# Optimization experiments

Hardware: AMD Instinct MI355X
Metric: run time of the kernel (lower is better)

## Reference

```python
import jax, jax.numpy as jnp
import numpy as np

B, S, H, E, K = 4, 2048, 1024, 8, 2

def setup_inputs() -> dict:
    key = jax.random.key(0)
    ks = jax.random.split(key, 7)
    scale = 1.0 / np.sqrt(H)
    return {
        "hidden_states": jax.random.normal(ks[0], (B, S, H), dtype=jnp.float32),
        "top_k_index": jax.random.randint(ks[1], (B, S, K), 0, E, dtype=jnp.int64),
        "top_k_weights": jax.random.uniform(ks[2], (B, S, K), dtype=jnp.float32),
        "w1": jax.random.normal(ks[3], (E, H, H), dtype=jnp.float32) * scale,
        "b1": jax.random.normal(ks[4], (E, H), dtype=jnp.float32) * scale,
        "w2": jax.random.normal(ks[5], (E, H, H), dtype=jnp.float32) * scale,
        "b2": jax.random.normal(ks[6], (E, H), dtype=jnp.float32) * scale,
    }

def reference(hidden_states, top_k_index, top_k_weights, w1, b1, w2, b2):
    # Per-token, per-expert combine weight: sum over k of tkw * (idx == e) -> [B,S,E]
    match = (top_k_index[..., None] == jnp.arange(E)[None, None, None, :])  # [B,S,K,E]
    comb = jnp.einsum("bsk,bske->bse", top_k_weights, match.astype(top_k_weights.dtype))
    # Dense per-expert FFN over ALL tokens (faithful to the naive module).
    h1 = jax.nn.relu(jnp.einsum("bsh,ehf->ebsf", hidden_states, w1) + b1[:, None, None, :])  # [E,B,S,H]
    h2 = jnp.einsum("ebsh,ehf->ebsf", h1, w2) + b2[:, None, None, :]  # [E,B,S,H]
    # Mask-weighted sum over experts.
    out = jnp.einsum("ebsh,bse->bsh", h2, comb)
    return out
```

## Files before the change

### kernel.cpp

```cpp
#include <hip/hip_runtime.h>
#include <hip/hip_bf16.h>
#include <stdint.h>

#define E_    8
#define H_    1024
#define NTOK  8192
#define KSEL  2
#define NSLOT (NTOK * KSEL)

typedef __attribute__((ext_vector_type(8))) short   short8_t;
typedef __attribute__((ext_vector_type(4))) float   f32x4;

#define BM 160
#define BN 128
#define BK 64
#define MAXMT 110
#define NT    (H_ / BN)
#define NWG   (MAXMT * NT)

#define CNT_OFF   0
#define TOK_OFF   1024
#define WSL_OFF   (TOK_OFF + NSLOT * 4)
#define XB_OFF    (1 << 18)
#define H1_OFF    (XB_OFF + (size_t)NTOK * H_ * 2)
#define W1T_OFF   (H1_OFF + (size_t)(NSLOT + 2048) * H_ * 2)
#define W2T_OFF   (W1T_OFF + (size_t)E_ * H_ * H_ * 2)

#define RT_T 1024
#define RT_S (NSLOT / RT_T)

__global__ __launch_bounds__(RT_T) void route_all(
    const int* __restrict__ idx, const float* __restrict__ tkw,
    int* __restrict__ cnt, int* __restrict__ tok, float* __restrict__ wsl) {
  __shared__ int hist[E_ * RT_T];
  const int t = threadIdx.x;
  const int p0 = t * RT_S;

  int myi[RT_S];
#pragma unroll
  for (int i = 0; i < RT_S; i += 4)
    *(int4*)&myi[i] = *(const int4*)&idx[p0 + i];
  int lc[E_];
#pragma unroll
  for (int j = 0; j < E_; ++j) lc[j] = 0;
#pragma unroll
  for (int i = 0; i < RT_S; ++i)
#pragma unroll
    for (int j = 0; j < E_; ++j) lc[j] += (myi[i] == j) ? 1 : 0;

#pragma unroll
  for (int j = 0; j < E_; ++j) hist[j * RT_T + t] = lc[j];
  __syncthreads();

  for (int s = 1; s < RT_T; s <<= 1) {
    int v[E_];
#pragma unroll
    for (int j = 0; j < E_; ++j) v[j] = (t >= s) ? hist[j * RT_T + (t - s)] : 0;
    __syncthreads();
#pragma unroll
    for (int j = 0; j < E_; ++j) hist[j * RT_T + t] += v[j];
    __syncthreads();
  }

  int tot[E_];
#pragma unroll
  for (int j = 0; j < E_; ++j) tot[j] = hist[j * RT_T + (RT_T - 1)];
  int base[E_];
  {
    int s = 0;
#pragma unroll
    for (int j = 0; j < E_; ++j) { base[j] = s; s += tot[j]; }
  }
  if (t < E_) cnt[t] = tot[t];

  int cur[E_];
#pragma unroll
  for (int j = 0; j < E_; ++j) cur[j] = base[j] + hist[j * RT_T + t] - lc[j];

  float myw[RT_S];
#pragma unroll
  for (int i = 0; i < RT_S; i += 4)
    *(float4*)&myw[i] = *(const float4*)&tkw[p0 + i];
#pragma unroll
  for (int i = 0; i < RT_S; ++i) {
    const int ev = myi[i];
    int pos = 0;
#pragma unroll
    for (int j = 0; j < E_; ++j)
      if (ev == j) { pos = cur[j]; cur[j] = pos + 1; }
    tok[pos] = (p0 + i) >> 1;
    wsl[pos] = myw[i];
  }
}

__global__ void xcast_zero(const float* __restrict__ x, __hip_bfloat16* __restrict__ xb,
                           float* __restrict__ out) {
  const size_t base = ((size_t)blockIdx.x * 256 + threadIdx.x) * 16;
  f32x4 z = f32x4{0.f, 0.f, 0.f, 0.f};
#pragma unroll
  for (int j = 0; j < 4; ++j) *(f32x4*)(out + base + j * 4) = z;
#pragma unroll
  for (int h = 0; h < 2; ++h) {
    f32x4 v0 = *(const f32x4*)(x + base + h * 8);
    f32x4 v1 = *(const f32x4*)(x + base + h * 8 + 4);
    union { __hip_bfloat16 b[8]; uint2 u[2]; } cv;
#pragma unroll
    for (int j = 0; j < 4; ++j) {
      cv.b[j]     = __float2bfloat16(v0[j]);
      cv.b[4 + j] = __float2bfloat16(v1[j]);
    }
    *(uint2*)(xb + base + h * 8)     = cv.u[0];
    *(uint2*)(xb + base + h * 8 + 4) = cv.u[1];
  }
}

__global__ void transpose_cast(const float* __restrict__ w1, const float* __restrict__ w2,
                               __hip_bfloat16* __restrict__ wt1, __hip_bfloat16* __restrict__ wt2) {
  __shared__ __hip_bfloat16 t[64][65];
  const int z = blockIdx.z;
  const float* W = (z < E_ ? w1 : w2) + ((size_t)(z & 7) << 20);
  __hip_bfloat16* WT = (z < E_ ? wt1 : wt2) + ((size_t)(z & 7) << 20);
  const int h0 = blockIdx.y * 64, f0 = blockIdx.x * 64;
  const int tid = threadIdx.x;
  const int tx = tid & 63, ty = tid >> 6;
#pragma unroll
  for (int i = 0; i < 16; ++i) {
    const int hl = i * 4 + ty;
    t[hl][tx] = __float2bfloat16(W[(size_t)(h0 + hl) * H_ + f0 + tx]);
  }
  __syncthreads();
  const int htx = tid & 15;
  const int fy  = tid >> 4;
#pragma unroll
  for (int j = 0; j < 4; ++j) {
    const int f = j * 16 + fy;
    union { __hip_bfloat16 h[4]; uint2 u; } v;
#pragma unroll
    for (int k = 0; k < 4; ++k) v.h[k] = t[htx * 4 + k][f];
    *reinterpret_cast<uint2*>(&WT[(size_t)(f0 + f) * H_ + h0 + htx * 4]) = v.u;
  }
}

#define FENCE_BAR() do {                                   \
    asm volatile("s_waitcnt lgkmcnt(0)" ::: "memory");     \
    __builtin_amdgcn_s_barrier();                          \
    __builtin_amdgcn_sched_barrier(0);                     \
  } while (0)

template <int EPI>
__launch_bounds__(256, 4)
__global__ void moe_gemm(const __hip_bfloat16* __restrict__ Asrc,
                         const __hip_bfloat16* __restrict__ Wt,
                         const float* __restrict__ bias,
                         __hip_bfloat16* __restrict__ h1out,
                         float* __restrict__ out,
                         const int* __restrict__ cnt,
                         const int* __restrict__ tok, const float* __restrict__ wsl) {
  const int wgid = (blockIdx.x & 7) * (NWG / 8) + (blockIdx.x >> 3);
  const int bt = wgid >> 3;
  const int nt = wgid & 7;

  int cn[E_];
#pragma unroll
  for (int i = 0; i < E_; ++i) cn[i] = cnt[i];
  int e = -1, mt = 0, count = 0, arow0 = 0;
  {
    int tacc = 0, sacc = 0;
#pragma unroll
    for (int i = 0; i < E_; ++i) {
      const int nti = (cn[i] + BM - 1) / BM;
      if (e < 0 && bt < tacc + nti) { e = i; mt = bt - tacc; count = cn[i]; arow0 = sacc + mt * BM; }
      tacc += nti; sacc += cn[i];
    }
  }
  if (e < 0) return;
  const size_t Arow0 = (size_t)arow0;

  const int tid = threadIdx.x;
  const int lane = tid & 63;
  const int wid = tid >> 6;
  const int wm = wid >> 1, wn = wid & 1;
  const int l15 = lane & 15, hi = lane >> 4, l7 = lane & 7;

  const __hip_bfloat16* Bexp = Wt + ((size_t)e << 20) + (size_t)(nt * BN) * H_;

  __shared__ __hip_bfloat16 smA[BM * BK];
  __shared__ __hip_bfloat16 smB[BN * BK];

  const int srow = tid >> 3;
  const int sun  = (tid & 7) * 8;
  const int swu  = (((tid & 7) ^ (srow & 7)) * 8);

  const __hip_bfloat16* aptr[5];
#pragma unroll
  for (int i = 0; i < 5; ++i) {
    if constexpr (EPI == 0) {
      int p = arow0 + i * 32 + srow;
      if (p > NSLOT - 1) p = NSLOT - 1;
      aptr[i] = Asrc + (size_t)tok[p] * H_ + sun;
    } else {
      aptr[i] = Asrc + (Arow0 + i * 32 + srow) * H_ + sun;
    }
  }
  const __hip_bfloat16* bptr = Bexp + (size_t)srow * H_ + sun;

  short8_t ra[5], rb[4];

  auto loadreg = [&](int kt) {
#pragma unroll
    for (int i = 0; i < 5; ++i)
      ra[i] = *(const short8_t*)(aptr[i] + kt * BK);
#pragma unroll
    for (int i = 0; i < 4; ++i)
      rb[i] = *(const short8_t*)(bptr + (size_t)(i * 32) * H_ + kt * BK);
  };
  auto dswrite = [&]() {
#pragma unroll
    for (int i = 0; i < 5; ++i)
      *(short8_t*)&smA[(i * 32 + srow) * BK + swu] = ra[i];
#pragma unroll
    for (int i = 0; i < 4; ++i)
      *(short8_t*)&smB[(i * 32 + srow) * BK + swu] = rb[i];
  };

  f32x4 acc[5][4];
#pragma unroll
  for (int mi = 0; mi < 5; ++mi)
#pragma unroll
    for (int ni = 0; ni < 4; ++ni) acc[mi][ni] = f32x4{0.f, 0.f, 0.f, 0.f};

  const int pu[2] = { ((0 * 4 + hi) ^ l7) * 8, ((1 * 4 + hi) ^ l7) * 8 };

  auto compute = [&]() {
#pragma unroll
    for (int ks = 0; ks < 2; ++ks) {
      short8_t a[5], b[4];
#pragma unroll
      for (int mi = 0; mi < 5; ++mi)
        a[mi] = *(const short8_t*)&smA[(wm * 80 + mi * 16 + l15) * BK + pu[ks]];
#pragma unroll
      for (int ni = 0; ni < 4; ++ni)
        b[ni] = *(const short8_t*)&smB[(wn * 64 + ni * 16 + l15) * BK + pu[ks]];
#pragma unroll
      for (int mi = 0; mi < 5; ++mi)
#pragma unroll
        for (int ni = 0; ni < 4; ++ni)
          acc[mi][ni] = __builtin_amdgcn_mfma_f32_16x16x32_bf16(a[mi], b[ni], acc[mi][ni], 0, 0, 0);
    }
  };

  const int KT = H_ / BK;

  loadreg(0);
  dswrite();
  FENCE_BAR();

  for (int kt = 0; kt < KT; ++kt) {
    if (kt + 1 < KT) loadreg(kt + 1);
    compute();
    if (kt + 1 < KT) {
      FENCE_BAR();
      dswrite();
      FENCE_BAR();
    }
  }

  const int colb = nt * BN + wn * 64;
  float bv[4];
#pragma unroll
  for (int ni = 0; ni < 4; ++ni) bv[ni] = bias[e * H_ + colb + ni * 16 + l15];

  if constexpr (EPI == 0) {
#pragma unroll
    for (int mi = 0; mi < 5; ++mi)
#pragma unroll
      for (int r = 0; r < 4; ++r) {
        const int lr = wm * 80 + mi * 16 + hi * 4 + r;
        if (mt * BM + lr < count) {
          __hip_bfloat16* rp = h1out + (Arow0 + lr) * H_ + colb;
#pragma unroll
          for (int ni = 0; ni < 4; ++ni) {
            float v = acc[mi][ni][r] + bv[ni];
            rp[ni * 16 + l15] = __float2bfloat16(fmaxf(v, 0.f));
          }
        }
      }
  } else {
#pragma unroll
    for (int mi = 0; mi < 5; ++mi)
#pragma unroll
      for (int r = 0; r < 4; ++r) {
        const int lr = wm * 80 + mi * 16 + hi * 4 + r;
        if (mt * BM + lr < count) {
          const int p = arow0 + lr;
          float* rp = out + (size_t)tok[p] * H_ + colb;
          const float w = wsl[p];
#pragma unroll
          for (int ni = 0; ni < 4; ++ni)
            atomicAdd(rp + ni * 16 + l15, (acc[mi][ni][r] + bv[ni]) * w);
        }
      }
  }
}

extern "C" void kernel_launch(void* const* d_in, const int* in_sizes, int n_in,
                              void* d_out, int out_size, void* d_ws, size_t ws_size,
                              hipStream_t stream) {
  const float* x   = (const float*)d_in[0];
  const int*   idx = (const int*)d_in[1];
  const float* tkw = (const float*)d_in[2];
  const float* w1  = (const float*)d_in[3];
  const float* b1  = (const float*)d_in[4];
  const float* w2  = (const float*)d_in[5];
  const float* b2  = (const float*)d_in[6];
  float* out = (float*)d_out;

  uint8_t* ws = (uint8_t*)d_ws;
  int*   cnt  = (int*)(ws + CNT_OFF);
  int*   tok  = (int*)(ws + TOK_OFF);
  float* wsl  = (float*)(ws + WSL_OFF);
  __hip_bfloat16* xb  = (__hip_bfloat16*)(ws + XB_OFF);
  __hip_bfloat16* h1  = (__hip_bfloat16*)(ws + H1_OFF);
  __hip_bfloat16* w1t = (__hip_bfloat16*)(ws + W1T_OFF);
  __hip_bfloat16* w2t = (__hip_bfloat16*)(ws + W2T_OFF);

  transpose_cast<<<dim3(H_ / 64, H_ / 64, 2 * E_), 256, 0, stream>>>(w1, w2, w1t, w2t);
  route_all<<<1, RT_T, 0, stream>>>(idx, tkw, cnt, tok, wsl);
  xcast_zero<<<NTOK * H_ / (256 * 16), 256, 0, stream>>>(x, xb, out);
  moe_gemm<0><<<NWG, 256, 0, stream>>>(xb, w1t, b1, h1, nullptr, cnt, tok, wsl);
  moe_gemm<1><<<NWG, 256, 0, stream>>>(h1, w2t, b2, nullptr, out, cnt, tok, wsl);
}
```

Baseline: 185.8 us.

## Drop LDS staging and load MFMA operands directly from global memory

Removes the shared-memory tiles, swizzled stores and barriers from the MoE GEMM. Each wave now loads its A and B MFMA fragments straight from global memory (through cache) inside a fully unrolled K loop. This removes LDS traffic and synchronisation, but operand reuse across waves now depends on L1/L2 instead of LDS, and each lane issues 16-byte loads strided by row, so global traffic and latency exposure go up.

```diff
diff --git a/kernel.cpp b/kernel.cpp
--- a/kernel.cpp
+++ b/kernel.cpp
@@ -13,7 +13,6 @@
 
 #define BM 160
 #define BN 128
-#define BK 64
 #define MAXMT 110
 #define NT    (H_ / BN)
 #define NWG   (MAXMT * NT)
@@ -140,12 +139,6 @@
     *reinterpret_cast<uint2*>(&WT[(size_t)(f0 + f) * H_ + h0 + htx * 4]) = v.u;
   }
 }
-
-#define FENCE_BAR() do {                                   \
-    asm volatile("s_waitcnt lgkmcnt(0)" ::: "memory");     \
-    __builtin_amdgcn_s_barrier();                          \
-    __builtin_amdgcn_sched_barrier(0);                     \
-  } while (0)
 
 template <int EPI>
 __launch_bounds__(256, 4)
@@ -180,48 +173,24 @@
   const int lane = tid & 63;
   const int wid = tid >> 6;
   const int wm = wid >> 1, wn = wid & 1;
-  const int l15 = lane & 15, hi = lane >> 4, l7 = lane & 7;
-
-  const __hip_bfloat16* Bexp = Wt + ((size_t)e << 20) + (size_t)(nt * BN) * H_;
-
-  __shared__ __hip_bfloat16 smA[BM * BK];
-  __shared__ __hip_bfloat16 smB[BN * BK];
-
-  const int srow = tid >> 3;
-  const int sun  = (tid & 7) * 8;
-  const int swu  = (((tid & 7) ^ (srow & 7)) * 8);
-
-  const __hip_bfloat16* aptr[5];
+  const int l15 = lane & 15, hi = lane >> 4;
+
+  const __hip_bfloat16* ap[5];
 #pragma unroll
   for (int i = 0; i < 5; ++i) {
+    const int row = arow0 + wm * 80 + i * 16 + l15;
     if constexpr (EPI == 0) {
-      int p = arow0 + i * 32 + srow;
+      int p = row;
       if (p > NSLOT - 1) p = NSLOT - 1;
-      aptr[i] = Asrc + (size_t)tok[p] * H_ + sun;
+      ap[i] = Asrc + (size_t)tok[p] * H_ + hi * 8;
     } else {
-      aptr[i] = Asrc + (Arow0 + i * 32 + srow) * H_ + sun;
-    }
-  }
-  const __hip_bfloat16* bptr = Bexp + (size_t)srow * H_ + sun;
-
-  short8_t ra[5], rb[4];
-
-  auto loadreg = [&](int kt) {
-#pragma unroll
-    for (int i = 0; i < 5; ++i)
-      ra[i] = *(const short8_t*)(aptr[i] + kt * BK);
-#pragma unroll
-    for (int i = 0; i < 4; ++i)
-      rb[i] = *(const short8_t*)(bptr + (size_t)(i * 32) * H_ + kt * BK);
-  };
-  auto dswrite = [&]() {
-#pragma unroll
-    for (int i = 0; i < 5; ++i)
-      *(short8_t*)&smA[(i * 32 + srow) * BK + swu] = ra[i];
-#pragma unroll
-    for (int i = 0; i < 4; ++i)
-      *(short8_t*)&smB[(i * 32 + srow) * BK + swu] = rb[i];
-  };
+      ap[i] = Asrc + (size_t)row * H_ + hi * 8;
+    }
+  }
+  const __hip_bfloat16* bp[4];
+#pragma unroll
+  for (int i = 0; i < 4; ++i)
+    bp[i] = Wt + ((size_t)e << 20) + (size_t)(nt * BN + wn * 64 + i * 16 + l15) * H_ + hi * 8;
 
   f32x4 acc[5][4];
 #pragma unroll
@@ -229,39 +198,23 @@
 #pragma unroll
     for (int ni = 0; ni < 4; ++ni) acc[mi][ni] = f32x4{0.f, 0.f, 0.f, 0.f};
 
-  const int pu[2] = { ((0 * 4 + hi) ^ l7) * 8, ((1 * 4 + hi) ^ l7) * 8 };
-
-  auto compute = [&]() {
+#pragma unroll
+  for (int kt = 0; kt < H_ / 64; ++kt) {
 #pragma unroll
     for (int ks = 0; ks < 2; ++ks) {
+      const int off = kt * 64 + ks * 32;
       short8_t a[5], b[4];
 #pragma unroll
       for (int mi = 0; mi < 5; ++mi)
-        a[mi] = *(const short8_t*)&smA[(wm * 80 + mi * 16 + l15) * BK + pu[ks]];
+        a[mi] = *(const short8_t*)(ap[mi] + off);
 #pragma unroll
       for (int ni = 0; ni < 4; ++ni)
-        b[ni] = *(const short8_t*)&smB[(wn * 64 + ni * 16 + l15) * BK + pu[ks]];
+        b[ni] = *(const short8_t*)(bp[ni] + off);
 #pragma unroll
       for (int mi = 0; mi < 5; ++mi)
 #pragma unroll
         for (int ni = 0; ni < 4; ++ni)
           acc[mi][ni] = __builtin_amdgcn_mfma_f32_16x16x32_bf16(a[mi], b[ni], acc[mi][ni], 0, 0, 0);
-    }
-  };
-
-  const int KT = H_ / BK;
-
-  loadreg(0);
-  dswrite();
-  FENCE_BAR();
-
-  for (int kt = 0; kt < KT; ++kt) {
-    if (kt + 1 < KT) loadreg(kt + 1);
-    compute();
-    if (kt + 1 < KT) {
-      FENCE_BAR();
-      dswrite();
-      FENCE_BAR();
     }
   }
 
```

Result: slower. 357.0 us (+92.2%).
